# Kernel optimization log

Measured on AMD Instinct MI355X. Metric: run time of the kernel, lower is better.

Reference implementation:

```python
import jax, jax.numpy as jnp
import numpy as np

NUM_LAYERS = 3
HIDDEN = 128
N_NODES = 50000
N_EDGES = 600000


def setup_inputs() -> dict:
    key = jax.random.key(0)
    ks = jax.random.split(key, 5)
    x = jax.random.normal(ks[0], (N_NODES, HIDDEN), dtype=jnp.float32)
    edge_index = jax.random.randint(ks[1], (2, N_EDGES), 0, N_NODES, dtype=jnp.int32)
    scale = 1.0 / np.sqrt(HIDDEN)
    # SAGEConv params per layer: lin_l (neighbor path, with bias), lin_r (root path, no bias)
    Wl = jax.random.uniform(ks[2], (NUM_LAYERS, HIDDEN, HIDDEN), jnp.float32, -scale, scale)
    bl = jnp.zeros((NUM_LAYERS, HIDDEN), dtype=jnp.float32)
    Wr = jax.random.uniform(ks[3], (NUM_LAYERS, HIDDEN, HIDDEN), jnp.float32, -scale, scale)
    return {"x": x, "edge_index": edge_index, "Wl": Wl, "bl": bl, "Wr": Wr}


def reference(x, edge_index, Wl, bl, Wr):
    # PyG SAGEConv (aggr='mean', root_weight=True):
    #   out = lin_l(mean_{j in N(i)} x_j) + lin_r(x_i)
    src = edge_index[0]
    dst = edge_index[1]
    n = x.shape[0]
    deg = jax.ops.segment_sum(jnp.ones(src.shape[0], dtype=x.dtype), dst, num_segments=n)
    inv_deg = (1.0 / jnp.maximum(deg, 1.0))[:, None]  # [N,1]
    h = x
    for i in range(NUM_LAYERS):
        agg = jax.ops.segment_sum(h[src], dst, num_segments=n) * inv_deg  # [N,H]
        h = agg @ Wl[i].T + bl[i] + h @ Wr[i].T
        if i < NUM_LAYERS - 1:
            h = jax.nn.relu(h)  # dropout_rate=0 -> Identity
    return h
```

## Files before the change

kernel.cpp:

```cpp
#include <hip/hip_runtime.h>
#include <hip/hip_bf16.h>

#define H 128

using bf16x8 = __attribute__((ext_vector_type(8))) short;
using f32x4  = __attribute__((ext_vector_type(4))) float;

__device__ inline unsigned short f2bf(float f) {
    unsigned u = __float_as_uint(f);
    unsigned r = (u + 0x7fffu + ((u >> 16) & 1u)) >> 16;
    return (unsigned short)r;
}
__device__ inline float bf2f(unsigned short b) {
    return __uint_as_float(((unsigned)b) << 16);
}


__global__ void k_zero_i32(int* __restrict__ p, int n) {
    int i = blockIdx.x * blockDim.x + threadIdx.x;
    if (i < n) p[i] = 0;
}

__global__ void k_count(const int* __restrict__ dst, int* __restrict__ deg, int e) {
    int i = blockIdx.x * blockDim.x + threadIdx.x;
    if (i < e) atomicAdd(&deg[dst[i]], 1);
}

__global__ __launch_bounds__(1024) void k_scan_partial(const int* __restrict__ deg,
                                                       int* __restrict__ partials, int n) {
    __shared__ int sm[1024];
    int t = threadIdx.x;
    int i = blockIdx.x * 1024 + t;
    sm[t] = (i < n) ? deg[i] : 0;
    __syncthreads();
    for (int s = 512; s > 0; s >>= 1) {
        if (t < s) sm[t] += sm[t + s];
        __syncthreads();
    }
    if (t == 0) partials[blockIdx.x] = sm[0];
}

__global__ __launch_bounds__(64) void k_scan_base(int* __restrict__ partials, int nb,
                                                  int* __restrict__ offsets, int n) {
    __shared__ int sm[64];
    int t = threadIdx.x;
    int v = (t < nb) ? partials[t] : 0;
    sm[t] = v;
    __syncthreads();
    for (int off = 1; off < 64; off <<= 1) {
        int x = 0;
        if (t >= off) x = sm[t - off];
        __syncthreads();
        if (t >= off) sm[t] += x;
        __syncthreads();
    }
    if (t < nb) partials[t] = sm[t] - v;
    if (t == 63) offsets[n] = sm[63];
}

__global__ __launch_bounds__(1024) void k_scan_final(const int* __restrict__ deg,
                                                     const int* __restrict__ partials,
                                                     int* __restrict__ offsets,
                                                     int* __restrict__ cursor,
                                                     float* __restrict__ inv_deg, int n) {
    __shared__ int sm[1024];
    int t = threadIdx.x;
    int b = blockIdx.x;
    int i = b * 1024 + t;
    int v = (i < n) ? deg[i] : 0;
    sm[t] = v;
    __syncthreads();
    for (int off = 1; off < 1024; off <<= 1) {
        int x = 0;
        if (t >= off) x = sm[t - off];
        __syncthreads();
        if (t >= off) sm[t] += x;
        __syncthreads();
    }
    if (i < n) {
        int excl = partials[b] + sm[t] - v;
        offsets[i] = excl;
        cursor[i]  = excl;
        inv_deg[i] = 1.0f / fmaxf((float)v, 1.0f);
    }
}

__global__ void k_fill(const int* __restrict__ src, const int* __restrict__ dst,
                       int* __restrict__ cursor, int* __restrict__ csr, int e) {
    int i = blockIdx.x * blockDim.x + threadIdx.x;
    if (i < e) {
        int d = dst[i];
        int pos = atomicAdd(&cursor[d], 1);
        csr[pos] = src[i];
    }
}

__global__ void k_wsplit(const float* __restrict__ Wl, const float* __restrict__ Wr,
                         unsigned short* __restrict__ Wf, int total) {
    int idx = blockIdx.x * blockDim.x + threadIdx.x;
    if (idx >= total) return;
    int l = idx >> 12;
    int rem = idx & 4095;
    int s = rem >> 9;
    int c = (rem >> 6) & 7;
    int lane = rem & 63;
    int j = c * 16 + (lane & 15);
    int k0 = s * 32 + (lane >> 4) * 8;
    size_t fc = (size_t)(idx >> 6);
    size_t hbase = (fc * 2 * 64 + lane) * 8;
    size_t lbase = hbase + 512;
    for (int jj = 0; jj < 8; ++jj) {
        int k = k0 + jj;
        float v;
        if (k < H) v = Wl[(size_t)l * H * H + j * H + k];
        else       v = Wr[(size_t)l * H * H + j * H + (k - H)];
        unsigned short hi = f2bf(v);
        unsigned short lo = f2bf(v - bf2f(hi));
        Wf[hbase + jj] = hi;
        Wf[lbase + jj] = lo;
    }
}


__global__ __launch_bounds__(256) void k_agg(const float* __restrict__ h,
                                             const int* __restrict__ csr,
                                             const int* __restrict__ offsets,
                                             const float* __restrict__ inv_deg,
                                             unsigned short* __restrict__ A_hi,
                                             unsigned short* __restrict__ A_lo, int n) {
    int node = blockIdx.x * 8 + (threadIdx.x >> 5);
    int l4 = threadIdx.x & 31;
    if (node >= n) return;
    int s = offsets[node];
    int eend = offsets[node + 1];
    const float4* hv = (const float4*)h;
    float4 a0 = make_float4(0.f, 0.f, 0.f, 0.f);
    float4 a1 = make_float4(0.f, 0.f, 0.f, 0.f);
    int p = s;
    for (; p + 1 < eend; p += 2) {
        int i0 = csr[p], i1 = csr[p + 1];
        float4 v0 = hv[(size_t)i0 * 32 + l4];
        float4 v1 = hv[(size_t)i1 * 32 + l4];
        a0.x += v0.x; a0.y += v0.y; a0.z += v0.z; a0.w += v0.w;
        a1.x += v1.x; a1.y += v1.y; a1.z += v1.z; a1.w += v1.w;
    }
    if (p < eend) {
        int i0 = csr[p];
        float4 v0 = hv[(size_t)i0 * 32 + l4];
        a0.x += v0.x; a0.y += v0.y; a0.z += v0.z; a0.w += v0.w;
    }
    float w = inv_deg[node];
    float4 acc;
    acc.x = (a0.x + a1.x) * w; acc.y = (a0.y + a1.y) * w;
    acc.z = (a0.z + a1.z) * w; acc.w = (a0.w + a1.w) * w;

    int tile = node >> 4;
    size_t base = ((size_t)(tile * 8 + (l4 >> 3)) * 64 + ((l4 >> 1) & 3) * 16 + (node & 15)) * 8
                  + (l4 & 1) * 4;

    ushort4 ahi, alo;
    ahi.x = f2bf(acc.x); alo.x = f2bf(acc.x - bf2f(ahi.x));
    ahi.y = f2bf(acc.y); alo.y = f2bf(acc.y - bf2f(ahi.y));
    ahi.z = f2bf(acc.z); alo.z = f2bf(acc.z - bf2f(ahi.z));
    ahi.w = f2bf(acc.w); alo.w = f2bf(acc.w - bf2f(ahi.w));
    *(ushort4*)(A_hi + base) = ahi;
    *(ushort4*)(A_lo + base) = alo;

    float4 hrow = hv[(size_t)node * 32 + l4];
    ushort4 hhi, hlo;
    hhi.x = f2bf(hrow.x); hlo.x = f2bf(hrow.x - bf2f(hhi.x));
    hhi.y = f2bf(hrow.y); hlo.y = f2bf(hrow.y - bf2f(hhi.y));
    hhi.z = f2bf(hrow.z); hlo.z = f2bf(hrow.z - bf2f(hhi.z));
    hhi.w = f2bf(hrow.w); hlo.w = f2bf(hrow.w - bf2f(hhi.w));
    *(ushort4*)(A_hi + base + 2048) = hhi;
    *(ushort4*)(A_lo + base + 2048) = hlo;
}

__global__ __launch_bounds__(256) void k_gemm_mfma(const unsigned short* __restrict__ A_hi,
                                                   const unsigned short* __restrict__ A_lo,
                                                   const unsigned short* __restrict__ Wf,
                                                   const float* __restrict__ bias,
                                                   float* __restrict__ out, int n, int relu,
                                                   int ntiles) {
    int wv = threadIdx.x >> 6;
    int lane = threadIdx.x & 63;
    int r16 = lane & 15;
    int kq = lane >> 4;
    int t0 = blockIdx.x * 8 + wv * 2;
    int t1 = t0 + 1;
    bool ok0 = t0 < ntiles;
    bool ok1 = t1 < ntiles;

    f32x4 acc[2][8];
#pragma unroll
    for (int t = 0; t < 2; ++t)
#pragma unroll
        for (int c = 0; c < 8; ++c) acc[t][c] = (f32x4){0.f, 0.f, 0.f, 0.f};

#pragma unroll
    for (int s = 0; s < 8; ++s) {
        bf16x8 a0h = {}, a0l = {}, a1h = {}, a1l = {};
        if (ok0) {
            size_t ab = ((size_t)(t0 * 8 + s) * 64 + lane) * 8;
            a0h = *(const bf16x8*)(A_hi + ab);
            a0l = *(const bf16x8*)(A_lo + ab);
        }
        if (ok1) {
            size_t ab = ((size_t)(t1 * 8 + s) * 64 + lane) * 8;
            a1h = *(const bf16x8*)(A_hi + ab);
            a1l = *(const bf16x8*)(A_lo + ab);
        }
#pragma unroll
        for (int c = 0; c < 8; ++c) {
            size_t wb = (((size_t)(s * 8 + c) * 2) * 64 + lane) * 8;
            bf16x8 b_hi = *(const bf16x8*)(Wf + wb);
            bf16x8 b_lo = *(const bf16x8*)(Wf + wb + 512);
            acc[0][c] = __builtin_amdgcn_mfma_f32_16x16x32_bf16(a0h, b_hi, acc[0][c], 0, 0, 0);
            acc[0][c] = __builtin_amdgcn_mfma_f32_16x16x32_bf16(a0h, b_lo, acc[0][c], 0, 0, 0);
            acc[0][c] = __builtin_amdgcn_mfma_f32_16x16x32_bf16(a0l, b_hi, acc[0][c], 0, 0, 0);
            acc[1][c] = __builtin_amdgcn_mfma_f32_16x16x32_bf16(a1h, b_hi, acc[1][c], 0, 0, 0);
            acc[1][c] = __builtin_amdgcn_mfma_f32_16x16x32_bf16(a1h, b_lo, acc[1][c], 0, 0, 0);
            acc[1][c] = __builtin_amdgcn_mfma_f32_16x16x32_bf16(a1l, b_hi, acc[1][c], 0, 0, 0);
        }
    }

#pragma unroll
    for (int t = 0; t < 2; ++t) {
        int tile = t ? t1 : t0;
        if (tile >= ntiles) continue;
#pragma unroll
        for (int c = 0; c < 8; ++c) {
            int col = c * 16 + r16;
            float b = bias[col];
#pragma unroll
            for (int r = 0; r < 4; ++r) {
                int grow = tile * 16 + kq * 4 + r;
                if (grow < n) {
                    float v = acc[t][c][r] + b;
                    if (relu) v = fmaxf(v, 0.f);
                    out[(size_t)grow * H + col] = v;
                }
            }
        }
    }
}


extern "C" void kernel_launch(void* const* d_in, const int* in_sizes, int n_in,
                              void* d_out, int out_size, void* d_ws, size_t ws_size,
                              hipStream_t stream) {
    const float* x  = (const float*)d_in[0];
    const int*   ei = (const int*)d_in[1];
    const float* Wl = (const float*)d_in[2];
    const float* bl = (const float*)d_in[3];
    const float* Wr = (const float*)d_in[4];
    float* out = (float*)d_out;

    int n = in_sizes[0] / H;
    int e = in_sizes[1] / 2;
    const int* srcp = ei;
    const int* dstp = ei + e;
    int ntiles = (n + 15) >> 4;

    char* w = (char*)d_ws;
    auto alloc = [&](size_t bytes) {
        char* p = w;
        w += (bytes + 255) & ~(size_t)255;
        return p;
    };
    int nb = (n + 1023) / 1024;
    int*            csr      = (int*)alloc((size_t)e * 4);
    int*            offsets  = (int*)alloc((size_t)(n + 1) * 4);
    int*            cursor   = (int*)alloc((size_t)n * 4);
    int*            deg      = (int*)alloc((size_t)n * 4);
    float*          inv_deg  = (float*)alloc((size_t)n * 4);
    int*            partials = (int*)alloc(64 * 4);
    unsigned short* Wf       = (unsigned short*)alloc((size_t)3 * 8 * 8 * 2 * 64 * 8 * 2);
    unsigned short* A_hi     = (unsigned short*)alloc((size_t)ntiles * 8 * 64 * 8 * 2);
    unsigned short* A_lo     = (unsigned short*)alloc((size_t)ntiles * 8 * 64 * 8 * 2);
    float*          hbuf     = (float*)alloc((size_t)n * H * 4);

    k_zero_i32<<<(n + 255) / 256, 256, 0, stream>>>(deg, n);
    k_count<<<(e + 255) / 256, 256, 0, stream>>>(dstp, deg, e);
    k_scan_partial<<<nb, 1024, 0, stream>>>(deg, partials, n);
    k_scan_base<<<1, 64, 0, stream>>>(partials, nb, offsets, n);
    k_scan_final<<<nb, 1024, 0, stream>>>(deg, partials, offsets, cursor, inv_deg, n);
    k_fill<<<(e + 255) / 256, 256, 0, stream>>>(srcp, dstp, cursor, csr, e);
    int wtot = 3 * 8 * 8 * 64;
    k_wsplit<<<(wtot + 255) / 256, 256, 0, stream>>>(Wl, Wr, Wf, wtot);

    const float* hin[3]  = {x, out, hbuf};
    float*       hout[3] = {out, hbuf, out};
    int gemm_grid = (ntiles + 7) / 8;
    for (int l = 0; l < 3; ++l) {
        k_agg<<<(n + 7) / 8, 256, 0, stream>>>(hin[l], csr, offsets, inv_deg, A_hi, A_lo, n);
        k_gemm_mfma<<<gemm_grid, 256, 0, stream>>>(A_hi, A_lo,
                                                   Wf + (size_t)l * 8 * 8 * 2 * 64 * 8,
                                                   bl + (size_t)l * H, hout[l], n,
                                                   l < 2 ? 1 : 0, ntiles);
    }
}
```

Baseline: 400.4 us.

## Fuse neighbor aggregation and MFMA GEMM into one kernel via LDS staging

Merges the per-layer aggregation kernel and the split-bf16 MFMA GEMM into a single kernel. Each block aggregates 64 nodes into LDS in MFMA fragment layout, then four waves each run one 16-row tile. The root-path half of A is converted from h directly in registers instead of being staged through global memory. This removes the global A_hi/A_lo round trip and one launch per layer. In exchange, each block now holds 32KB of LDS, the gather loop is unrolled to four edges, each wave handles one tile instead of two, and gather and GEMM phases no longer overlap across kernels.

After: 485.0 us. 21.1% more time.

```diff
diff --git a/kernel.cpp b/kernel.cpp
--- a/kernel.cpp
+++ b/kernel.cpp
@@ -121,125 +121,140 @@
     }
 }
 
-
-__global__ __launch_bounds__(256) void k_agg(const float* __restrict__ h,
-                                             const int* __restrict__ csr,
-                                             const int* __restrict__ offsets,
-                                             const float* __restrict__ inv_deg,
-                                             unsigned short* __restrict__ A_hi,
-                                             unsigned short* __restrict__ A_lo, int n) {
-    int node = blockIdx.x * 8 + (threadIdx.x >> 5);
-    int l4 = threadIdx.x & 31;
-    if (node >= n) return;
-    int s = offsets[node];
-    int eend = offsets[node + 1];
-    const float4* hv = (const float4*)h;
-    float4 a0 = make_float4(0.f, 0.f, 0.f, 0.f);
-    float4 a1 = make_float4(0.f, 0.f, 0.f, 0.f);
-    int p = s;
-    for (; p + 1 < eend; p += 2) {
-        int i0 = csr[p], i1 = csr[p + 1];
-        float4 v0 = hv[(size_t)i0 * 32 + l4];
-        float4 v1 = hv[(size_t)i1 * 32 + l4];
-        a0.x += v0.x; a0.y += v0.y; a0.z += v0.z; a0.w += v0.w;
-        a1.x += v1.x; a1.y += v1.y; a1.z += v1.z; a1.w += v1.w;
-    }
-    if (p < eend) {
-        int i0 = csr[p];
-        float4 v0 = hv[(size_t)i0 * 32 + l4];
-        a0.x += v0.x; a0.y += v0.y; a0.z += v0.z; a0.w += v0.w;
-    }
-    float w = inv_deg[node];
-    float4 acc;
-    acc.x = (a0.x + a1.x) * w; acc.y = (a0.y + a1.y) * w;
-    acc.z = (a0.z + a1.z) * w; acc.w = (a0.w + a1.w) * w;
-
-    int tile = node >> 4;
-    size_t base = ((size_t)(tile * 8 + (l4 >> 3)) * 64 + ((l4 >> 1) & 3) * 16 + (node & 15)) * 8
-                  + (l4 & 1) * 4;
-
-    ushort4 ahi, alo;
-    ahi.x = f2bf(acc.x); alo.x = f2bf(acc.x - bf2f(ahi.x));
-    ahi.y = f2bf(acc.y); alo.y = f2bf(acc.y - bf2f(ahi.y));
-    ahi.z = f2bf(acc.z); alo.z = f2bf(acc.z - bf2f(ahi.z));
-    ahi.w = f2bf(acc.w); alo.w = f2bf(acc.w - bf2f(ahi.w));
-    *(ushort4*)(A_hi + base) = ahi;
-    *(ushort4*)(A_lo + base) = alo;
-
-    float4 hrow = hv[(size_t)node * 32 + l4];
-    ushort4 hhi, hlo;
-    hhi.x = f2bf(hrow.x); hlo.x = f2bf(hrow.x - bf2f(hhi.x));
-    hhi.y = f2bf(hrow.y); hlo.y = f2bf(hrow.y - bf2f(hhi.y));
-    hhi.z = f2bf(hrow.z); hlo.z = f2bf(hrow.z - bf2f(hhi.z));
-    hhi.w = f2bf(hrow.w); hlo.w = f2bf(hrow.w - bf2f(hhi.w));
-    *(ushort4*)(A_hi + base + 2048) = hhi;
-    *(ushort4*)(A_lo + base + 2048) = hlo;
-}
-
-__global__ __launch_bounds__(256) void k_gemm_mfma(const unsigned short* __restrict__ A_hi,
-                                                   const unsigned short* __restrict__ A_lo,
-                                                   const unsigned short* __restrict__ Wf,
-                                                   const float* __restrict__ bias,
-                                                   float* __restrict__ out, int n, int relu,
-                                                   int ntiles) {
-    int wv = threadIdx.x >> 6;
-    int lane = threadIdx.x & 63;
+__global__ __launch_bounds__(256) void k_fused(const float* __restrict__ h,
+                                               const int* __restrict__ csr,
+                                               const int* __restrict__ offsets,
+                                               const float* __restrict__ inv_deg,
+                                               const unsigned short* __restrict__ Wf,
+                                               const float* __restrict__ bias,
+                                               float* __restrict__ out, int n, int relu) {
+    __shared__ unsigned short AL[16384];
+
+    int t = threadIdx.x;
+
+    {
+        int grp = t >> 5;
+        int l4 = t & 31;
+        const float4* hv = (const float4*)h;
+        for (int i = 0; i < 8; ++i) {
+            int bn = grp * 8 + i;
+            int gnode = blockIdx.x * 64 + bn;
+            if (gnode >= n) break;
+            int ps = offsets[gnode];
+            int pe = offsets[gnode + 1];
+            float4 a0 = make_float4(0.f, 0.f, 0.f, 0.f);
+            float4 a1 = make_float4(0.f, 0.f, 0.f, 0.f);
+            float4 a2 = make_float4(0.f, 0.f, 0.f, 0.f);
+            float4 a3 = make_float4(0.f, 0.f, 0.f, 0.f);
+            int p = ps;
+            for (; p + 3 < pe; p += 4) {
+                int i0 = csr[p], i1 = csr[p + 1], i2 = csr[p + 2], i3 = csr[p + 3];
+                float4 v0 = hv[(size_t)i0 * 32 + l4];
+                float4 v1 = hv[(size_t)i1 * 32 + l4];
+                float4 v2 = hv[(size_t)i2 * 32 + l4];
+                float4 v3 = hv[(size_t)i3 * 32 + l4];
+                a0.x += v0.x; a0.y += v0.y; a0.z += v0.z; a0.w += v0.w;
+                a1.x += v1.x; a1.y += v1.y; a1.z += v1.z; a1.w += v1.w;
+                a2.x += v2.x; a2.y += v2.y; a2.z += v2.z; a2.w += v2.w;
+                a3.x += v3.x; a3.y += v3.y; a3.z += v3.z; a3.w += v3.w;
+            }
+            for (; p < pe; ++p) {
+                int i0 = csr[p];
+                float4 v0 = hv[(size_t)i0 * 32 + l4];
+                a0.x += v0.x; a0.y += v0.y; a0.z += v0.z; a0.w += v0.w;
+            }
+            float w = inv_deg[gnode];
+            float4 acc;
+            acc.x = ((a0.x + a1.x) + (a2.x + a3.x)) * w;
+            acc.y = ((a0.y + a1.y) + (a2.y + a3.y)) * w;
+            acc.z = ((a0.z + a1.z) + (a2.z + a3.z)) * w;
+            acc.w = ((a0.w + a1.w) + (a2.w + a3.w)) * w;
+
+            int tile = bn >> 4, r16 = bn & 15;
+            int s = l4 >> 3;
+            int kq = (l4 >> 1) & 3;
+            int e0 = (l4 & 1) * 4;
+            int offh = (((tile * 4 + s) * 2 + 0) * 64 + kq * 16 + r16) * 8 + e0;
+            int offl = offh + 512;
+
+            ushort4 hi4, lo4;
+            hi4.x = f2bf(acc.x); lo4.x = f2bf(acc.x - bf2f(hi4.x));
+            hi4.y = f2bf(acc.y); lo4.y = f2bf(acc.y - bf2f(hi4.y));
+            hi4.z = f2bf(acc.z); lo4.z = f2bf(acc.z - bf2f(hi4.z));
+            hi4.w = f2bf(acc.w); lo4.w = f2bf(acc.w - bf2f(hi4.w));
+            *(ushort4*)(&AL[offh]) = hi4;
+            *(ushort4*)(&AL[offl]) = lo4;
+        }
+    }
+    __syncthreads();
+
+    int wv = t >> 6;
+    int lane = t & 63;
     int r16 = lane & 15;
     int kq = lane >> 4;
-    int t0 = blockIdx.x * 8 + wv * 2;
-    int t1 = t0 + 1;
-    bool ok0 = t0 < ntiles;
-    bool ok1 = t1 < ntiles;
-
-    f32x4 acc[2][8];
-#pragma unroll
-    for (int t = 0; t < 2; ++t)
-#pragma unroll
-        for (int c = 0; c < 8; ++c) acc[t][c] = (f32x4){0.f, 0.f, 0.f, 0.f};
-
-#pragma unroll
-    for (int s = 0; s < 8; ++s) {
-        bf16x8 a0h = {}, a0l = {}, a1h = {}, a1l = {};
-        if (ok0) {
-            size_t ab = ((size_t)(t0 * 8 + s) * 64 + lane) * 8;
-            a0h = *(const bf16x8*)(A_hi + ab);
-            a0l = *(const bf16x8*)(A_lo + ab);
-        }
-        if (ok1) {
-            size_t ab = ((size_t)(t1 * 8 + s) * 64 + lane) * 8;
-            a1h = *(const bf16x8*)(A_hi + ab);
-            a1l = *(const bf16x8*)(A_lo + ab);
-        }
+    int tile_g = blockIdx.x * 4 + wv;
+
+    f32x4 acc[8];
+#pragma unroll
+    for (int c = 0; c < 8; ++c) acc[c] = (f32x4){0.f, 0.f, 0.f, 0.f};
+
+#pragma unroll
+    for (int s = 0; s < 4; ++s) {
+        int ab = (((wv * 4 + s) * 2) * 64 + lane) * 8;
+        bf16x8 ah = *(const bf16x8*)(&AL[ab]);
+        bf16x8 al = *(const bf16x8*)(&AL[ab + 512]);
 #pragma unroll
         for (int c = 0; c < 8; ++c) {
             size_t wb = (((size_t)(s * 8 + c) * 2) * 64 + lane) * 8;
             bf16x8 b_hi = *(const bf16x8*)(Wf + wb);
             bf16x8 b_lo = *(const bf16x8*)(Wf + wb + 512);
-            acc[0][c] = __builtin_amdgcn_mfma_f32_16x16x32_bf16(a0h, b_hi, acc[0][c], 0, 0, 0);
-            acc[0][c] = __builtin_amdgcn_mfma_f32_16x16x32_bf16(a0h, b_lo, acc[0][c], 0, 0, 0);
-            acc[0][c] = __builtin_amdgcn_mfma_f32_16x16x32_bf16(a0l, b_hi, acc[0][c], 0, 0, 0);
-            acc[1][c] = __builtin_amdgcn_mfma_f32_16x16x32_bf16(a1h, b_hi, acc[1][c], 0, 0, 0);
-            acc[1][c] = __builtin_amdgcn_mfma_f32_16x16x32_bf16(a1h, b_lo, acc[1][c], 0, 0, 0);
-            acc[1][c] = __builtin_amdgcn_mfma_f32_16x16x32_bf16(a1l, b_hi, acc[1][c], 0, 0, 0);
-        }
-    }
-
-#pragma unroll
-    for (int t = 0; t < 2; ++t) {
-        int tile = t ? t1 : t0;
-        if (tile >= ntiles) continue;
+            acc[c] = __builtin_amdgcn_mfma_f32_16x16x32_bf16(ah, b_hi, acc[c], 0, 0, 0);
+            acc[c] = __builtin_amdgcn_mfma_f32_16x16x32_bf16(ah, b_lo, acc[c], 0, 0, 0);
+            acc[c] = __builtin_amdgcn_mfma_f32_16x16x32_bf16(al, b_hi, acc[c], 0, 0, 0);
+        }
+    }
+
+    int grow = tile_g * 16 + r16;
+    bool rok = grow < n;
+#pragma unroll
+    for (int s = 4; s < 8; ++s) {
+        bf16x8 ah = {}, al = {};
+        if (rok) {
+            const float* hp = h + (size_t)grow * H + (s - 4) * 32 + kq * 8;
+            float4 v0 = *(const float4*)hp;
+            float4 v1 = *(const float4*)(hp + 4);
+            unsigned short x;
+            x = f2bf(v0.x); ah[0] = (short)x; al[0] = (short)f2bf(v0.x - bf2f(x));
+            x = f2bf(v0.y); ah[1] = (short)x; al[1] = (short)f2bf(v0.y - bf2f(x));
+            x = f2bf(v0.z); ah[2] = (short)x; al[2] = (short)f2bf(v0.z - bf2f(x));
+            x = f2bf(v0.w); ah[3] = (short)x; al[3] = (short)f2bf(v0.w - bf2f(x));
+            x = f2bf(v1.x); ah[4] = (short)x; al[4] = (short)f2bf(v1.x - bf2f(x));
+            x = f2bf(v1.y); ah[5] = (short)x; al[5] = (short)f2bf(v1.y - bf2f(x));
+            x = f2bf(v1.z); ah[6] = (short)x; al[6] = (short)f2bf(v1.z - bf2f(x));
+            x = f2bf(v1.w); ah[7] = (short)x; al[7] = (short)f2bf(v1.w - bf2f(x));
+        }
 #pragma unroll
         for (int c = 0; c < 8; ++c) {
-            int col = c * 16 + r16;
-            float b = bias[col];
-#pragma unroll
-            for (int r = 0; r < 4; ++r) {
-                int grow = tile * 16 + kq * 4 + r;
-                if (grow < n) {
-                    float v = acc[t][c][r] + b;
-                    if (relu) v = fmaxf(v, 0.f);
-                    out[(size_t)grow * H + col] = v;
-                }
+            size_t wb = (((size_t)(s * 8 + c) * 2) * 64 + lane) * 8;
+            bf16x8 b_hi = *(const bf16x8*)(Wf + wb);
+            bf16x8 b_lo = *(const bf16x8*)(Wf + wb + 512);
+            acc[c] = __builtin_amdgcn_mfma_f32_16x16x32_bf16(ah, b_hi, acc[c], 0, 0, 0);
+            acc[c] = __builtin_amdgcn_mfma_f32_16x16x32_bf16(ah, b_lo, acc[c], 0, 0, 0);
+            acc[c] = __builtin_amdgcn_mfma_f32_16x16x32_bf16(al, b_hi, acc[c], 0, 0, 0);
+        }
+    }
+
+#pragma unroll
+    for (int c = 0; c < 8; ++c) {
+        int col = c * 16 + r16;
+        float b = bias[col];
+#pragma unroll
+        for (int r = 0; r < 4; ++r) {
+            int go = tile_g * 16 + kq * 4 + r;
+            if (go < n) {
+                float v = acc[c][r] + b;
+                if (relu) v = fmaxf(v, 0.f);
+                out[(size_t)go * H + col] = v;
             }
         }
     }
@@ -260,7 +275,6 @@
     int e = in_sizes[1] / 2;
     const int* srcp = ei;
     const int* dstp = ei + e;
-    int ntiles = (n + 15) >> 4;
 
     char* w = (char*)d_ws;
     auto alloc = [&](size_t bytes) {
@@ -276,8 +290,6 @@
     float*          inv_deg  = (float*)alloc((size_t)n * 4);
     int*            partials = (int*)alloc(64 * 4);
     unsigned short* Wf       = (unsigned short*)alloc((size_t)3 * 8 * 8 * 2 * 64 * 8 * 2);
-    unsigned short* A_hi     = (unsigned short*)alloc((size_t)ntiles * 8 * 64 * 8 * 2);
-    unsigned short* A_lo     = (unsigned short*)alloc((size_t)ntiles * 8 * 64 * 8 * 2);
     float*          hbuf     = (float*)alloc((size_t)n * H * 4);
 
     k_zero_i32<<<(n + 255) / 256, 256, 0, stream>>>(deg, n);
@@ -291,12 +303,10 @@
 
     const float* hin[3]  = {x, out, hbuf};
     float*       hout[3] = {out, hbuf, out};
-    int gemm_grid = (ntiles + 7) / 8;
+    int nblk = (n + 63) / 64;
     for (int l = 0; l < 3; ++l) {
-        k_agg<<<(n + 7) / 8, 256, 0, stream>>>(hin[l], csr, offsets, inv_deg, A_hi, A_lo, n);
-        k_gemm_mfma<<<gemm_grid, 256, 0, stream>>>(A_hi, A_lo,
-                                                   Wf + (size_t)l * 8 * 8 * 2 * 64 * 8,
-                                                   bl + (size_t)l * H, hout[l], n,
-                                                   l < 2 ? 1 : 0, ntiles);
-    }
-}
+        k_fused<<<nblk, 256, 0, stream>>>(hin[l], csr, offsets, inv_deg,
+                                          Wf + (size_t)l * 8 * 8 * 2 * 64 * 8,
+                                          bl + (size_t)l * H, hout[l], n, l < 2 ? 1 : 0);
+    }
+}
```
